# Performance work log

Hardware: AMD Instinct MI355X
Metric: run time of the kernel (lower is better)

The kernel has to match this reference:

```python
import jax, jax.numpy as jnp
import numpy as np

B, H, W, C = 8, 64, 64, 128
BN_EPS = 1e-3  # keras BatchNormalization default epsilon


def setup_inputs() -> dict:
    key = jax.random.key(0)
    ks = jax.random.split(key, 8)
    scale = 1.0 / np.sqrt(C)
    return {
        "x": jax.random.normal(ks[0], (B, H, W, C), dtype=jnp.float32),
        "wq": jax.random.normal(ks[1], (C, C), dtype=jnp.float32) * scale,
        "bq": jnp.zeros((C,), dtype=jnp.float32),
        "wk": jax.random.normal(ks[2], (C, C), dtype=jnp.float32) * scale,
        "bk": jnp.zeros((C,), dtype=jnp.float32),
        "wv": jax.random.normal(ks[3], (C, C), dtype=jnp.float32) * scale,
        "bv": jnp.zeros((C,), dtype=jnp.float32),
        "gamma": jnp.ones((C,), dtype=jnp.float32),
        "beta": jnp.zeros((C,), dtype=jnp.float32),
        "mov_mean": jax.random.normal(ks[4], (C,), dtype=jnp.float32) * 0.1,
        "mov_var": jax.random.uniform(ks[5], (C,), dtype=jnp.float32) * 0.5 + 0.5,
    }


def reference(x, wq, bq, wk, bk, wv, bv, gamma, beta, mov_mean, mov_var):
    b, h, w, c = x.shape
    n = h * w
    # 1x1 convs == per-pixel linear projections
    q = (jnp.einsum('bhwc,cd->bhwd', x, wq) + bq).reshape(b, n, c)
    k = (jnp.einsum('bhwc,cd->bhwd', x, wk) + bk).reshape(b, n, c)
    v = (jnp.einsum('bhwc,cd->bhwd', x, wv) + bv).reshape(b, n, c)
    # full [n, n] attention matrix (as in the original module)
    scores = jnp.einsum('bnc,bmc->bnm', q, k) / jnp.sqrt(jnp.asarray(c, x.dtype))
    attn = jax.nn.softmax(scores, axis=-1)  # dropout is identity in inference
    out = jnp.einsum('bnm,bmc->bnc', attn, v).reshape(b, h, w, c)
    out = out + x  # residual
    # BatchNormalization, inference mode (moving statistics)
    inv = gamma * jax.lax.rsqrt(mov_var + BN_EPS)
    out = out * inv + (beta - mov_mean * inv)
    return out
```

## Files before the change

### kernel.cpp

```cpp
#include <hip/hip_runtime.h>


typedef __attribute__((ext_vector_type(8))) short bf16x8;
typedef __attribute__((ext_vector_type(4))) float f32x4;

__device__ __forceinline__ unsigned short f2bf(float f) {
  unsigned int u = __builtin_bit_cast(unsigned int, f);
  u += 0x7fffu + ((u >> 16) & 1u);
  return (unsigned short)(u >> 16);
}
__device__ __forceinline__ unsigned int pack2(float a, float b) {
  return (unsigned int)f2bf(a) | ((unsigned int)f2bf(b) << 16);
}

#define SCALE_Q (0.08838834764831845f * 1.44269504088896340f)

__global__ void prep_wt(const float* __restrict__ wq, const float* __restrict__ wk,
                        const float* __restrict__ wv, unsigned short* __restrict__ wt) {
  const float* W = (blockIdx.x == 0) ? wq : (blockIdx.x == 1 ? wk : wv);
  const float sc = (blockIdx.x == 0) ? SCALE_Q : 1.0f;
  unsigned short* out = wt + blockIdx.x * 16384;
  int id = blockIdx.y * 256 + threadIdx.x;
  int n  = id >> 5;
  int kb = (id & 31) * 4;
#pragma unroll
  for (int k = 0; k < 4; ++k)
    out[n * 128 + kb + k] = f2bf(W[(kb + k) * 128 + n] * sc);
}

__global__ __launch_bounds__(256) void qkv_fused(
    const float* __restrict__ x, const unsigned short* __restrict__ wt,
    const float* __restrict__ bq, const float* __restrict__ bk, const float* __restrict__ bv,
    unsigned short* __restrict__ Qg, unsigned short* __restrict__ Kg,
    unsigned short* __restrict__ Vtg) {
  __shared__ unsigned short xs[128 * 128];
  __shared__ unsigned short vlds[128 * 136];
  const int t = threadIdx.x;
  const int rowblk = blockIdx.x * 128;

#pragma unroll
  for (int i = 0; i < 16; ++i) {
    int flat = t * 4 + i * 1024;
    int row = flat >> 7, col = flat & 127;
    float4 v = *(const float4*)(x + (size_t)(rowblk + row) * 128 + col);
    unsigned int u0 = pack2(v.x, v.y), u1 = pack2(v.z, v.w);
    int pos = (col >> 3) ^ (row & 15);
    *(uint2*)(xs + row * 128 + pos * 8 + (col & 7)) = make_uint2(u0, u1);
  }
  __syncthreads();

  const int lane = t & 63, wv_ = t >> 6;
  const int lm = lane & 15, quad = lane >> 4;

  bf16x8 a[2][4];
#pragma unroll
  for (int tr = 0; tr < 2; ++tr) {
    int row = wv_ * 32 + tr * 16 + lm;
#pragma unroll
    for (int ks = 0; ks < 4; ++ks)
      a[tr][ks] = __builtin_bit_cast(bf16x8,
          *(const uint4*)(xs + row * 128 + (((ks * 4 + quad) ^ lm) * 8)));
  }

  const f32x4 zero4 = {0.f, 0.f, 0.f, 0.f};
#pragma unroll 1
  for (int p = 0; p < 3; ++p) {
    const unsigned short* w = wt + p * 16384;
    const float* bias = (p == 0) ? bq : (p == 1 ? bk : bv);
    const float bsc = (p == 0) ? SCALE_Q : 1.0f;

    f32x4 acc[2][8];
#pragma unroll
    for (int tr = 0; tr < 2; ++tr)
#pragma unroll
      for (int ct = 0; ct < 8; ++ct) acc[tr][ct] = zero4;

#pragma unroll
    for (int ct = 0; ct < 8; ++ct) {
      int n = ct * 16 + lm;
      const uint4* wp = (const uint4*)(w + n * 128 + quad * 8);
#pragma unroll
      for (int ks = 0; ks < 4; ++ks) {
        bf16x8 bfr = __builtin_bit_cast(bf16x8, wp[ks * 4]);
        acc[0][ct] = __builtin_amdgcn_mfma_f32_16x16x32_bf16(a[0][ks], bfr, acc[0][ct], 0, 0, 0);
        acc[1][ct] = __builtin_amdgcn_mfma_f32_16x16x32_bf16(a[1][ks], bfr, acc[1][ct], 0, 0, 0);
      }
    }

    if (p < 2) {
      unsigned short* og = (p == 0) ? Qg : Kg;
#pragma unroll
      for (int tr = 0; tr < 2; ++tr) {
        int rowb = rowblk + wv_ * 32 + tr * 16 + quad * 4;
#pragma unroll
        for (int ct = 0; ct < 8; ++ct) {
          int c = ct * 16 + lm;
          float bb = bias[c] * bsc;
#pragma unroll
          for (int r = 0; r < 4; ++r)
            og[(size_t)(rowb + r) * 128 + c] = f2bf(acc[tr][ct][r] + bb);
        }
      }
    } else {
#pragma unroll
      for (int tr = 0; tr < 2; ++tr) {
        int key_base = wv_ * 32 + tr * 16 + quad * 4;
#pragma unroll
        for (int ct = 0; ct < 8; ++ct) {
          int c = ct * 16 + lm;
          float bb = bias[c];
          unsigned int u0 = pack2(acc[tr][ct][0] + bb, acc[tr][ct][1] + bb);
          unsigned int u1 = pack2(acc[tr][ct][2] + bb, acc[tr][ct][3] + bb);
          *(uint2*)(vlds + (size_t)c * 136 + key_base) = make_uint2(u0, u1);
        }
      }
      __syncthreads();
      int c2 = t >> 1;
      int ch = (t & 1) * 8;
      int b  = rowblk >> 12;
      int nb0 = rowblk & 4095;
#pragma unroll
      for (int j = 0; j < 8; ++j) {
        uint4 vv = *(const uint4*)(vlds + (size_t)c2 * 136 + (ch + j) * 8);
        *(uint4*)(Vtg + (size_t)b * 524288 + (size_t)c2 * 4096 + nb0 + (ch + j) * 8) = vv;
      }
    }
  }
}

__global__ __launch_bounds__(256, 2) void flash_attn(
    const unsigned short* __restrict__ Qg, const unsigned short* __restrict__ Kg,
    const unsigned short* __restrict__ Vtg, const float* __restrict__ x,
    const float* __restrict__ gamma, const float* __restrict__ beta,
    const float* __restrict__ mmean, const float* __restrict__ mvar,
    float* __restrict__ out) {
  __shared__ uint4 Pb[2048];
  __shared__ float lred[256];

  const int b  = blockIdx.x & 7;
  const int qt = blockIdx.x >> 3;
  const int t = threadIdx.x;
  const int lane = t & 63;
  const int w = t >> 6;
  const int lm = lane & 15, quad = lane >> 4;
  const int q0 = qt * 64;

  const unsigned short* Qb = Qg  + (size_t)b * 524288;
  const unsigned short* Kb = Kg  + (size_t)b * 524288;
  const unsigned short* Vb = Vtg + (size_t)b * 524288;

  bf16x8 qf[4][4];
#pragma unroll
  for (int nt = 0; nt < 4; ++nt) {
    const uint4* qp = (const uint4*)(Qb + (size_t)(q0 + nt * 16 + lm) * 128 + quad * 8);
#pragma unroll
    for (int ks = 0; ks < 4; ++ks) qf[nt][ks] = __builtin_bit_cast(bf16x8, qp[ks * 4]);
  }

  const f32x4 zero4 = {0.f, 0.f, 0.f, 0.f};
  f32x4 o[2][4];
#pragma unroll
  for (int mt = 0; mt < 2; ++mt)
#pragma unroll
    for (int nt = 0; nt < 4; ++nt) o[mt][nt] = zero4;
  float lp[4] = {0.f, 0.f, 0.f, 0.f};

  for (int kt = 0; kt < 32; ++kt) {
    const int key0 = kt * 128;

    bf16x8 kf[2][4], vf[2][4];
#pragma unroll
    for (int mt = 0; mt < 2; ++mt) {
      const uint4* kp = (const uint4*)(Kb + (size_t)(key0 + w * 32 + mt * 16 + lm) * 128 + quad * 8);
      const uint4* vp = (const uint4*)(Vb + (size_t)(w * 32 + mt * 16 + lm) * 4096 + key0 + quad * 8);
#pragma unroll
      for (int ks = 0; ks < 4; ++ks) {
        kf[mt][ks] = __builtin_bit_cast(bf16x8, kp[ks * 4]);
        vf[mt][ks] = __builtin_bit_cast(bf16x8, vp[ks * 4]);
      }
    }

    f32x4 sa[2][4];
#pragma unroll
    for (int mt = 0; mt < 2; ++mt)
#pragma unroll
      for (int nt = 0; nt < 4; ++nt) sa[mt][nt] = zero4;
#pragma unroll
    for (int ks = 0; ks < 4; ++ks)
#pragma unroll
      for (int mt = 0; mt < 2; ++mt)
#pragma unroll
        for (int nt = 0; nt < 4; ++nt)
          sa[mt][nt] = __builtin_amdgcn_mfma_f32_16x16x32_bf16(kf[mt][ks], qf[nt][ks], sa[mt][nt], 0, 0, 0);

    unsigned short* Ps = (unsigned short*)(Pb + (kt & 1) * 1024);
    const int sub = (quad & 1) * 4;
#pragma unroll
    for (int mt = 0; mt < 2; ++mt) {
      int c16 = w * 4 + mt * 2 + (quad >> 1);
      int pos = c16 ^ lm;
#pragma unroll
      for (int nt = 0; nt < 4; ++nt) {
        float e0 = exp2f(sa[mt][nt][0]), e1 = exp2f(sa[mt][nt][1]);
        float e2 = exp2f(sa[mt][nt][2]), e3 = exp2f(sa[mt][nt][3]);
        lp[nt] += (e0 + e1) + (e2 + e3);
        *(uint2*)(Ps + (nt * 16 + lm) * 128 + pos * 8 + sub) =
            make_uint2(pack2(e0, e1), pack2(e2, e3));
      }
    }
    __syncthreads();

    const uint4* Pr = Pb + (kt & 1) * 1024;
#pragma unroll
    for (int nt = 0; nt < 4; ++nt) {
      bf16x8 pf[4];
#pragma unroll
      for (int ks = 0; ks < 4; ++ks)
        pf[ks] = __builtin_bit_cast(bf16x8, Pr[(nt * 16 + lm) * 16 + ((ks * 4 + quad) ^ lm)]);
#pragma unroll
      for (int ks = 0; ks < 4; ++ks)
#pragma unroll
        for (int mt = 0; mt < 2; ++mt)
          o[mt][nt] = __builtin_amdgcn_mfma_f32_16x16x32_bf16(vf[mt][ks], pf[ks], o[mt][nt], 0, 0, 0);
    }
  }

#pragma unroll
  for (int nt = 0; nt < 4; ++nt) {
    lp[nt] += __shfl_xor(lp[nt], 16);
    lp[nt] += __shfl_xor(lp[nt], 32);
  }
  if (quad == 0) {
#pragma unroll
    for (int nt = 0; nt < 4; ++nt) lred[w * 64 + nt * 16 + lm] = lp[nt];
  }
  __syncthreads();
  float rl[4];
#pragma unroll
  for (int nt = 0; nt < 4; ++nt) {
    int q = nt * 16 + lm;
    rl[nt] = 1.0f / ((lred[q] + lred[64 + q]) + (lred[128 + q] + lred[192 + q]));
  }

#pragma unroll
  for (int mt = 0; mt < 2; ++mt) {
    int c0 = w * 32 + mt * 16 + quad * 4;
    float4 gm = *(const float4*)(gamma + c0);
    float4 bt = *(const float4*)(beta + c0);
    float4 mm = *(const float4*)(mmean + c0);
    float4 mv = *(const float4*)(mvar + c0);
    float iv0 = gm.x * rsqrtf(mv.x + 1e-3f), iv1 = gm.y * rsqrtf(mv.y + 1e-3f);
    float iv2 = gm.z * rsqrtf(mv.z + 1e-3f), iv3 = gm.w * rsqrtf(mv.w + 1e-3f);
    float ad0 = bt.x - mm.x * iv0, ad1 = bt.y - mm.y * iv1;
    float ad2 = bt.z - mm.z * iv2, ad3 = bt.w - mm.w * iv3;
#pragma unroll
    for (int nt = 0; nt < 4; ++nt) {
      size_t g = ((size_t)b * 4096 + q0 + nt * 16 + lm) * 128 + c0;
      float4 xr = *(const float4*)(x + g);
      float4 ov;
      ov.x = (o[mt][nt][0] * rl[nt] + xr.x) * iv0 + ad0;
      ov.y = (o[mt][nt][1] * rl[nt] + xr.y) * iv1 + ad1;
      ov.z = (o[mt][nt][2] * rl[nt] + xr.z) * iv2 + ad2;
      ov.w = (o[mt][nt][3] * rl[nt] + xr.w) * iv3 + ad3;
      *(float4*)(out + g) = ov;
    }
  }
}

extern "C" void kernel_launch(void* const* d_in, const int* in_sizes, int n_in,
                              void* d_out, int out_size, void* d_ws, size_t ws_size,
                              hipStream_t stream) {
  const float* x     = (const float*)d_in[0];
  const float* wq    = (const float*)d_in[1];
  const float* bq    = (const float*)d_in[2];
  const float* wk    = (const float*)d_in[3];
  const float* bk    = (const float*)d_in[4];
  const float* wv    = (const float*)d_in[5];
  const float* bv    = (const float*)d_in[6];
  const float* gamma = (const float*)d_in[7];
  const float* beta  = (const float*)d_in[8];
  const float* mmean = (const float*)d_in[9];
  const float* mvar  = (const float*)d_in[10];
  float* out = (float*)d_out;

  unsigned short* wt  = (unsigned short*)d_ws;
  unsigned short* Qg  = wt + 3 * 128 * 128;
  unsigned short* Kg  = Qg + 8 * 4096 * 128;
  unsigned short* Vtg = Kg + 8 * 4096 * 128;

  prep_wt<<<dim3(3, 16), dim3(256), 0, stream>>>(wq, wk, wv, wt);
  qkv_fused<<<dim3(256), dim3(256), 0, stream>>>(x, wt, bq, bk, bv, Qg, Kg, Vtg);
  flash_attn<<<dim3(512), dim3(256), 0, stream>>>(Qg, Kg, Vtg, x, gamma, beta, mmean, mvar, out);
}
```

Measured before the change: 233.4 us.

## Stage K tiles in LDS via async global-to-LDS DMA and split QKV projection grid

The attention kernel now double-buffers each 128-key K tile in shared memory, filling it with global_load_lds DMA while the P·V stage runs, instead of loading K fragments straight from global memory into registers. K is written pre-swizzled by the projection kernel so the LDS reads avoid bank conflicts. The projection kernel is split across a 3-wide grid dimension (one projection per block, 64 rows) with coalesced stores staged through LDS. This adds 64KB of LDS per attention block, which may limit occupancy below the requested two blocks per CU. It also puts an extra barrier in every iteration.

```diff
diff --git a/kernel.cpp b/kernel.cpp
--- a/kernel.cpp
+++ b/kernel.cpp
@@ -11,6 +11,12 @@
 }
 __device__ __forceinline__ unsigned int pack2(float a, float b) {
   return (unsigned int)f2bf(a) | ((unsigned int)f2bf(b) << 16);
+}
+
+__device__ __forceinline__ void dma16(const void* g, void* l) {
+  __builtin_amdgcn_global_load_lds(
+      (const __attribute__((address_space(1))) unsigned int*)g,
+      (__attribute__((address_space(3))) unsigned int*)l, 16, 0, 0);
 }
 
 #define SCALE_Q (0.08838834764831845f * 1.44269504088896340f)
@@ -28,18 +34,19 @@
     out[n * 128 + kb + k] = f2bf(W[(kb + k) * 128 + n] * sc);
 }
 
-__global__ __launch_bounds__(256) void qkv_fused(
+__global__ __launch_bounds__(256) void qkv_proj(
     const float* __restrict__ x, const unsigned short* __restrict__ wt,
     const float* __restrict__ bq, const float* __restrict__ bk, const float* __restrict__ bv,
     unsigned short* __restrict__ Qg, unsigned short* __restrict__ Kg,
     unsigned short* __restrict__ Vtg) {
-  __shared__ unsigned short xs[128 * 128];
-  __shared__ unsigned short vlds[128 * 136];
+  __shared__ unsigned short xs[64 * 128];
+  __shared__ unsigned short obuf[9216];
   const int t = threadIdx.x;
-  const int rowblk = blockIdx.x * 128;
-
-#pragma unroll
-  for (int i = 0; i < 16; ++i) {
+  const int p = blockIdx.y;
+  const int rowblk = blockIdx.x * 64;
+
+#pragma unroll
+  for (int i = 0; i < 8; ++i) {
     int flat = t * 4 + i * 1024;
     int row = flat >> 7, col = flat & 127;
     float4 v = *(const float4*)(x + (size_t)(rowblk + row) * 128 + col);
@@ -52,78 +59,75 @@
   const int lane = t & 63, wv_ = t >> 6;
   const int lm = lane & 15, quad = lane >> 4;
 
-  bf16x8 a[2][4];
-#pragma unroll
-  for (int tr = 0; tr < 2; ++tr) {
-    int row = wv_ * 32 + tr * 16 + lm;
+  bf16x8 a[4];
+  {
+    int row = wv_ * 16 + lm;
 #pragma unroll
     for (int ks = 0; ks < 4; ++ks)
-      a[tr][ks] = __builtin_bit_cast(bf16x8,
+      a[ks] = __builtin_bit_cast(bf16x8,
           *(const uint4*)(xs + row * 128 + (((ks * 4 + quad) ^ lm) * 8)));
   }
 
+  const unsigned short* w = wt + p * 16384;
+  const float* bias = (p == 0) ? bq : (p == 1 ? bk : bv);
+  const float bsc = (p == 0) ? SCALE_Q : 1.0f;
+
   const f32x4 zero4 = {0.f, 0.f, 0.f, 0.f};
-#pragma unroll 1
-  for (int p = 0; p < 3; ++p) {
-    const unsigned short* w = wt + p * 16384;
-    const float* bias = (p == 0) ? bq : (p == 1 ? bk : bv);
-    const float bsc = (p == 0) ? SCALE_Q : 1.0f;
-
-    f32x4 acc[2][8];
-#pragma unroll
-    for (int tr = 0; tr < 2; ++tr)
-#pragma unroll
-      for (int ct = 0; ct < 8; ++ct) acc[tr][ct] = zero4;
-
+  f32x4 acc[8];
+#pragma unroll
+  for (int ct = 0; ct < 8; ++ct) acc[ct] = zero4;
+
+#pragma unroll
+  for (int ct = 0; ct < 8; ++ct) {
+    int n = ct * 16 + lm;
+    const uint4* wp = (const uint4*)(w + n * 128 + quad * 8);
+#pragma unroll
+    for (int ks = 0; ks < 4; ++ks) {
+      bf16x8 bfr = __builtin_bit_cast(bf16x8, wp[ks * 4]);
+      acc[ct] = __builtin_amdgcn_mfma_f32_16x16x32_bf16(a[ks], bfr, acc[ct], 0, 0, 0);
+    }
+  }
+
+  const int b   = rowblk >> 12;
+  const int nb0 = rowblk & 4095;
+
+  if (p < 2) {
+    int rowb = wv_ * 16 + quad * 4;
 #pragma unroll
     for (int ct = 0; ct < 8; ++ct) {
-      int n = ct * 16 + lm;
-      const uint4* wp = (const uint4*)(w + n * 128 + quad * 8);
-#pragma unroll
-      for (int ks = 0; ks < 4; ++ks) {
-        bf16x8 bfr = __builtin_bit_cast(bf16x8, wp[ks * 4]);
-        acc[0][ct] = __builtin_amdgcn_mfma_f32_16x16x32_bf16(a[0][ks], bfr, acc[0][ct], 0, 0, 0);
-        acc[1][ct] = __builtin_amdgcn_mfma_f32_16x16x32_bf16(a[1][ks], bfr, acc[1][ct], 0, 0, 0);
-      }
-    }
-
-    if (p < 2) {
-      unsigned short* og = (p == 0) ? Qg : Kg;
-#pragma unroll
-      for (int tr = 0; tr < 2; ++tr) {
-        int rowb = rowblk + wv_ * 32 + tr * 16 + quad * 4;
-#pragma unroll
-        for (int ct = 0; ct < 8; ++ct) {
-          int c = ct * 16 + lm;
-          float bb = bias[c] * bsc;
-#pragma unroll
-          for (int r = 0; r < 4; ++r)
-            og[(size_t)(rowb + r) * 128 + c] = f2bf(acc[tr][ct][r] + bb);
-        }
-      }
-    } else {
-#pragma unroll
-      for (int tr = 0; tr < 2; ++tr) {
-        int key_base = wv_ * 32 + tr * 16 + quad * 4;
-#pragma unroll
-        for (int ct = 0; ct < 8; ++ct) {
-          int c = ct * 16 + lm;
-          float bb = bias[c];
-          unsigned int u0 = pack2(acc[tr][ct][0] + bb, acc[tr][ct][1] + bb);
-          unsigned int u1 = pack2(acc[tr][ct][2] + bb, acc[tr][ct][3] + bb);
-          *(uint2*)(vlds + (size_t)c * 136 + key_base) = make_uint2(u0, u1);
-        }
-      }
-      __syncthreads();
-      int c2 = t >> 1;
-      int ch = (t & 1) * 8;
-      int b  = rowblk >> 12;
-      int nb0 = rowblk & 4095;
-#pragma unroll
-      for (int j = 0; j < 8; ++j) {
-        uint4 vv = *(const uint4*)(vlds + (size_t)c2 * 136 + (ch + j) * 8);
-        *(uint4*)(Vtg + (size_t)b * 524288 + (size_t)c2 * 4096 + nb0 + (ch + j) * 8) = vv;
-      }
+      int c = ct * 16 + lm;
+      float bb = bias[c] * bsc;
+#pragma unroll
+      for (int r = 0; r < 4; ++r)
+        obuf[(rowb + r) * 136 + c] = f2bf(acc[ct][r] + bb);
+    }
+    __syncthreads();
+    unsigned short* og = (p == 0) ? Qg : Kg;
+    int row = t >> 2;
+#pragma unroll
+    for (int j = 0; j < 4; ++j) {
+      int ch = (t & 3) * 4 + j;
+      int pos = (p == 1) ? (ch ^ (row & 15)) : ch;
+      uint4 vv = *(const uint4*)(obuf + row * 136 + ch * 8);
+      *(uint4*)(og + (size_t)(rowblk + row) * 128 + pos * 8) = vv;
+    }
+  } else {
+    int key_base = wv_ * 16 + quad * 4;
+#pragma unroll
+    for (int ct = 0; ct < 8; ++ct) {
+      int c = ct * 16 + lm;
+      float bb = bias[c];
+      unsigned int u0 = pack2(acc[ct][0] + bb, acc[ct][1] + bb);
+      unsigned int u1 = pack2(acc[ct][2] + bb, acc[ct][3] + bb);
+      *(uint2*)(obuf + c * 72 + key_base) = make_uint2(u0, u1);
+    }
+    __syncthreads();
+    int d = t >> 1;
+#pragma unroll
+    for (int j = 0; j < 4; ++j) {
+      int ch = (t & 1) * 4 + j;
+      uint4 vv = *(const uint4*)(obuf + d * 72 + ch * 8);
+      *(uint4*)(Vtg + (size_t)b * 524288 + (size_t)d * 4096 + nb0 + ch * 8) = vv;
     }
   }
 }
@@ -134,8 +138,8 @@
     const float* __restrict__ gamma, const float* __restrict__ beta,
     const float* __restrict__ mmean, const float* __restrict__ mvar,
     float* __restrict__ out) {
-  __shared__ uint4 Pb[2048];
-  __shared__ float lred[256];
+  __shared__ unsigned short Kt[2][16384];
+  __shared__ unsigned short Pbuf[8192];
 
   const int b  = blockIdx.x & 7;
   const int qt = blockIdx.x >> 3;
@@ -165,66 +169,91 @@
     for (int nt = 0; nt < 4; ++nt) o[mt][nt] = zero4;
   float lp[4] = {0.f, 0.f, 0.f, 0.f};
 
+  {
+    const unsigned short* src = Kb + (size_t)w * 4096 + lane * 8;
+    unsigned short* dst = &Kt[0][w * 4096];
+#pragma unroll
+    for (int j = 0; j < 8; ++j) dma16(src + j * 512, dst + j * 512);
+  }
+  __syncthreads();
+
+#pragma unroll 1
   for (int kt = 0; kt < 32; ++kt) {
+    const int bi = kt & 1;
     const int key0 = kt * 128;
 
-    bf16x8 kf[2][4], vf[2][4];
+    bf16x8 vf[2][4];
 #pragma unroll
     for (int mt = 0; mt < 2; ++mt) {
-      const uint4* kp = (const uint4*)(Kb + (size_t)(key0 + w * 32 + mt * 16 + lm) * 128 + quad * 8);
       const uint4* vp = (const uint4*)(Vb + (size_t)(w * 32 + mt * 16 + lm) * 4096 + key0 + quad * 8);
 #pragma unroll
-      for (int ks = 0; ks < 4; ++ks) {
-        kf[mt][ks] = __builtin_bit_cast(bf16x8, kp[ks * 4]);
-        vf[mt][ks] = __builtin_bit_cast(bf16x8, vp[ks * 4]);
+      for (int ks = 0; ks < 4; ++ks) vf[mt][ks] = __builtin_bit_cast(bf16x8, vp[ks * 4]);
+    }
+
+    f32x4 sa[2][4];
+#pragma unroll
+    for (int mt = 0; mt < 2; ++mt)
+#pragma unroll
+      for (int nt = 0; nt < 4; ++nt) sa[mt][nt] = zero4;
+#pragma unroll
+    for (int mt = 0; mt < 2; ++mt) {
+      const unsigned short* kr = &Kt[bi][(w * 32 + mt * 16 + lm) * 128];
+      bf16x8 kf[4];
+#pragma unroll
+      for (int ks = 0; ks < 4; ++ks)
+        kf[ks] = __builtin_bit_cast(bf16x8, *(const uint4*)(kr + ((ks * 4 + quad) ^ lm) * 8));
+#pragma unroll
+      for (int ks = 0; ks < 4; ++ks)
+#pragma unroll
+        for (int nt = 0; nt < 4; ++nt)
+          sa[mt][nt] = __builtin_amdgcn_mfma_f32_16x16x32_bf16(kf[ks], qf[nt][ks], sa[mt][nt], 0, 0, 0);
+    }
+
+    {
+      unsigned short* Ps = Pbuf;
+      const int sub = (quad & 1) * 4;
+#pragma unroll
+      for (int mt = 0; mt < 2; ++mt) {
+        int c16 = w * 4 + mt * 2 + (quad >> 1);
+        int pos = c16 ^ lm;
+#pragma unroll
+        for (int nt = 0; nt < 4; ++nt) {
+          float e0 = exp2f(sa[mt][nt][0]), e1 = exp2f(sa[mt][nt][1]);
+          float e2 = exp2f(sa[mt][nt][2]), e3 = exp2f(sa[mt][nt][3]);
+          lp[nt] += (e0 + e1) + (e2 + e3);
+          *(uint2*)(Ps + (nt * 16 + lm) * 128 + pos * 8 + sub) =
+              make_uint2(pack2(e0, e1), pack2(e2, e3));
+        }
       }
     }
-
-    f32x4 sa[2][4];
-#pragma unroll
-    for (int mt = 0; mt < 2; ++mt)
-#pragma unroll
-      for (int nt = 0; nt < 4; ++nt) sa[mt][nt] = zero4;
-#pragma unroll
-    for (int ks = 0; ks < 4; ++ks)
-#pragma unroll
-      for (int mt = 0; mt < 2; ++mt)
-#pragma unroll
-        for (int nt = 0; nt < 4; ++nt)
-          sa[mt][nt] = __builtin_amdgcn_mfma_f32_16x16x32_bf16(kf[mt][ks], qf[nt][ks], sa[mt][nt], 0, 0, 0);
-
-    unsigned short* Ps = (unsigned short*)(Pb + (kt & 1) * 1024);
-    const int sub = (quad & 1) * 4;
-#pragma unroll
-    for (int mt = 0; mt < 2; ++mt) {
-      int c16 = w * 4 + mt * 2 + (quad >> 1);
-      int pos = c16 ^ lm;
+    __syncthreads();
+
+    if (kt + 1 < 32) {
+      const unsigned short* src = Kb + (size_t)(kt + 1) * 16384 + w * 4096 + lane * 8;
+      unsigned short* dst = &Kt[bi ^ 1][w * 4096];
+#pragma unroll
+      for (int j = 0; j < 8; ++j) dma16(src + j * 512, dst + j * 512);
+    }
+
+    {
+      const uint4* Pr = (const uint4*)Pbuf;
 #pragma unroll
       for (int nt = 0; nt < 4; ++nt) {
-        float e0 = exp2f(sa[mt][nt][0]), e1 = exp2f(sa[mt][nt][1]);
-        float e2 = exp2f(sa[mt][nt][2]), e3 = exp2f(sa[mt][nt][3]);
-        lp[nt] += (e0 + e1) + (e2 + e3);
-        *(uint2*)(Ps + (nt * 16 + lm) * 128 + pos * 8 + sub) =
-            make_uint2(pack2(e0, e1), pack2(e2, e3));
+        bf16x8 pf[4];
+#pragma unroll
+        for (int ks = 0; ks < 4; ++ks)
+          pf[ks] = __builtin_bit_cast(bf16x8, Pr[(nt * 16 + lm) * 16 + ((ks * 4 + quad) ^ lm)]);
+#pragma unroll
+        for (int ks = 0; ks < 4; ++ks)
+#pragma unroll
+          for (int mt = 0; mt < 2; ++mt)
+            o[mt][nt] = __builtin_amdgcn_mfma_f32_16x16x32_bf16(vf[mt][ks], pf[ks], o[mt][nt], 0, 0, 0);
       }
     }
     __syncthreads();
-
-    const uint4* Pr = Pb + (kt & 1) * 1024;
-#pragma unroll
-    for (int nt = 0; nt < 4; ++nt) {
-      bf16x8 pf[4];
-#pragma unroll
-      for (int ks = 0; ks < 4; ++ks)
-        pf[ks] = __builtin_bit_cast(bf16x8, Pr[(nt * 16 + lm) * 16 + ((ks * 4 + quad) ^ lm)]);
-#pragma unroll
-      for (int ks = 0; ks < 4; ++ks)
-#pragma unroll
-        for (int mt = 0; mt < 2; ++mt)
-          o[mt][nt] = __builtin_amdgcn_mfma_f32_16x16x32_bf16(vf[mt][ks], pf[ks], o[mt][nt], 0, 0, 0);
-    }
-  }
-
+  }
+
+  float* lred = (float*)Pbuf;
 #pragma unroll
   for (int nt = 0; nt < 4; ++nt) {
     lp[nt] += __shfl_xor(lp[nt], 16);
@@ -289,6 +318,7 @@
   unsigned short* Vtg = Kg + 8 * 4096 * 128;
 
   prep_wt<<<dim3(3, 16), dim3(256), 0, stream>>>(wq, wk, wv, wt);
-  qkv_fused<<<dim3(256), dim3(256), 0, stream>>>(x, wt, bq, bk, bv, Qg, Kg, Vtg);
-  flash_attn<<<dim3(512), dim3(256), 0, stream>>>(Qg, Kg, Vtg, x, gamma, beta, mmean, mvar, out);
-}
+  qkv_proj<<<dim3(512, 3), dim3(256), 0, stream>>>(x, wt, bq, bk, bv, Qg, Kg, Vtg);
+  flash_attn<<<dim3(512), dim3(256), 0, stream>>>(Qg, Kg, Vtg, x, gamma, beta,
+                                                  mmean, mvar, out);
+}
```

Result: faster. 218.1 us (-6.6%).
